# Performance work log

Hardware: AMD Instinct MI355X
Metric: run time of the kernel (lower is better)

Reference implementation:

```python
import jax, jax.numpy as jnp
import numpy as np

DIM = 512          # model dim
K = 4              # max_block_size (depthwise conv kernel size)
DS = 4             # downsample_factor
BLOCKS = (1, 2, 3, 4)  # block sizes, all offset 0
MULT = 12          # lcm(1,2,3,4) = block_pad_multiple
VOCAB = 256


def setup_inputs() -> dict:
    key = jax.random.key(0)
    ks = jax.random.split(key, 7)
    x = jax.random.randint(ks[0], (4, 4096), 0, VOCAB)
    emb = jax.random.normal(ks[1], (VOCAB, DIM), dtype=jnp.float32) * 0.02
    dw_w = jax.random.normal(ks[2], (DIM, 1, K), dtype=jnp.float32) * 0.1   # depthwise conv weight [out, in/groups, k]
    dw_b = jnp.zeros((DIM,), dtype=jnp.float32)
    pw_w = jax.random.normal(ks[3], (DIM, DIM), dtype=jnp.float32) * 0.05   # 1x1 conv weight [out, in]
    pw_b = jnp.zeros((DIM,), dtype=jnp.float32)
    score_w = jax.random.normal(ks[4], (DIM,), dtype=jnp.float32) * 0.05    # Linear(dim,1)
    score_b = jnp.zeros((), dtype=jnp.float32)
    return {"x": x, "emb": emb, "dw_w": dw_w, "dw_b": dw_b,
            "pw_w": pw_w, "pw_b": pw_b, "score_w": score_w, "score_b": score_b}


def _gbst(x, emb, dw_w, dw_b, pw_w, pw_b, score_w, score_b):
    b, n = x.shape
    m = ((n + DS - 1) // DS) * DS  # next multiple of downsample factor
    xe = emb[x]  # [b, n, d]

    # positional: Pad seq end by K-1, depthwise conv1d(k=K), then 1x1 conv
    xp = jnp.pad(xe, ((0, 0), (0, K - 1), (0, 0)))
    xc = jnp.transpose(xp, (0, 2, 1))  # [b, d, n+K-1]
    y = jax.lax.conv_general_dilated(
        xc, dw_w, window_strides=(1,), padding='VALID',
        dimension_numbers=('NCH', 'OIH', 'NCH'), feature_group_count=DIM)
    y = y + dw_b[None, :, None]                       # [b, d, n]
    y = jnp.einsum('ed,bdn->bne', pw_w, y) + pw_b     # [b, n, d]

    # pad seq to multiple of lcm of block sizes
    L = ((n + MULT - 1) // MULT) * MULT
    xpad = jnp.pad(y, ((0, 0), (0, L - n), (0, 0)))   # [b, L, d]

    # multi-scale block mean pooling, broadcast back to full length
    reprs = []
    for bs in BLOCKS:
        br = xpad.reshape(b, L // bs, bs, DIM).mean(axis=2)  # [b, L/bs, d]
        reprs.append(jnp.repeat(br, bs, axis=1))             # [b, L, d]
    block_reprs = jnp.stack(reprs, axis=2)  # [b, L, nblocks, d]

    # learned block scoring + softmax over block sizes
    scores = jnp.einsum('blkd,d->blk', block_reprs, score_w) + score_b
    scores = jax.nn.softmax(scores, axis=2)  # [b, L, nblocks]

    # consensus attention over positions (inner dim = nblocks)
    sim = jnp.einsum('bik,bjk->bij', scores, scores)  # [b, L, L]
    attn = jax.nn.softmax(sim, axis=-1)
    scores = jnp.einsum('bij,bjk->bik', attn, scores)

    out = jnp.einsum('blkd,blk->bld', block_reprs, scores)  # [b, L, d]
    out = out[:, :m]
    out = out.reshape(b, m // DS, DS, DIM).mean(axis=2)     # [b, m/DS, d]
    return out


def reference(x, emb, dw_w, dw_b, pw_w, pw_b, score_w, score_b):
    return _gbst(x, emb, dw_w, dw_b, pw_w, pw_b, score_w, score_b)
```

## Files before the change

kernel.cpp:

```cpp
#include <hip/hip_runtime.h>
#include <hip/hip_bf16.h>

#define DIMD 512
#define NSEQ 4096
#define LPAD 4104
#define NCH 12
#define CH 342
#define SPLITS 8
#define PT_BK 32

#define OFF_P      0u
#define OFF_CONST  524288u
#define OFF_T      524800u
#define OFF_S      541216u
#define OFF_AACC   606880u
#define OFF_Y      672544u
#define OFF_PPART  2773792u

static __device__ __forceinline__ unsigned short f2bf(float f) {
  unsigned u = __float_as_uint(f);
  unsigned r = (u + 0x7FFFu + ((u >> 16) & 1u)) >> 16;
  return (unsigned short)r;
}
static __device__ __forceinline__ float bf2f(unsigned short h) {
  return __uint_as_float(((unsigned)h) << 16);
}

__global__ __launch_bounds__(256) void k_ptable(
    const float* __restrict__ emb, const float* __restrict__ dw_w,
    const float* __restrict__ pw_w, float* __restrict__ Ppart) {
  __shared__ float As[PT_BK][68];
  __shared__ float Bs[PT_BK][68];
  const int tid = threadIdx.x;
  const int m0 = blockIdx.x * 64;
  const int e0 = blockIdx.y * 64;
  const int z  = blockIdx.z;
  const int kk = m0 >> 8;
  const int v0 = m0 & 255;
  const int srow = tid >> 3;
  const int sd4  = (tid & 7) * 4;
  const int ty = tid >> 4, tx = tid & 15;
  float c[4][4] = {};
  for (int kt = 0; kt < 64; kt += PT_BK) {
    const int d0 = z * 64 + kt;
    const float dw0 = dw_w[(d0 + sd4 + 0) * 4 + kk];
    const float dw1 = dw_w[(d0 + sd4 + 1) * 4 + kk];
    const float dw2 = dw_w[(d0 + sd4 + 2) * 4 + kk];
    const float dw3 = dw_w[(d0 + sd4 + 3) * 4 + kk];
    #pragma unroll
    for (int rr = 0; rr < 2; ++rr) {
      const int row = srow + rr * 32;
      float4 ev = *reinterpret_cast<const float4*>(&emb[(v0 + row) * DIMD + d0 + sd4]);
      As[sd4 + 0][row] = ev.x * dw0;
      As[sd4 + 1][row] = ev.y * dw1;
      As[sd4 + 2][row] = ev.z * dw2;
      As[sd4 + 3][row] = ev.w * dw3;
      float4 bv = *reinterpret_cast<const float4*>(&pw_w[(e0 + row) * DIMD + d0 + sd4]);
      Bs[sd4 + 0][row] = bv.x;
      Bs[sd4 + 1][row] = bv.y;
      Bs[sd4 + 2][row] = bv.z;
      Bs[sd4 + 3][row] = bv.w;
    }
    __syncthreads();
    #pragma unroll
    for (int q = 0; q < PT_BK; ++q) {
      float4 a = *reinterpret_cast<const float4*>(&As[q][ty * 4]);
      float4 b = *reinterpret_cast<const float4*>(&Bs[q][tx * 4]);
      c[0][0] += a.x * b.x; c[0][1] += a.x * b.y; c[0][2] += a.x * b.z; c[0][3] += a.x * b.w;
      c[1][0] += a.y * b.x; c[1][1] += a.y * b.y; c[1][2] += a.y * b.z; c[1][3] += a.y * b.w;
      c[2][0] += a.z * b.x; c[2][1] += a.z * b.y; c[2][2] += a.z * b.z; c[2][3] += a.z * b.w;
      c[3][0] += a.w * b.x; c[3][1] += a.w * b.y; c[3][2] += a.w * b.z; c[3][3] += a.w * b.w;
    }
    __syncthreads();
  }
  #pragma unroll
  for (int i = 0; i < 4; ++i) {
    *reinterpret_cast<float4*>(
        &Ppart[(size_t)z * 524288u + (m0 + ty * 4 + i) * DIMD + e0 + tx * 4]) =
        make_float4(c[i][0], c[i][1], c[i][2], c[i][3]);
  }
}

__global__ __launch_bounds__(256) void k_pcomb(
    const float* __restrict__ Ppart, float* __restrict__ P,
    const float* __restrict__ pw_w, const float* __restrict__ pw_b,
    const float* __restrict__ dw_b, float* __restrict__ constv) {
  const int idx = blockIdx.x * 256 + threadIdx.x;
  const float4* p4 = reinterpret_cast<const float4*>(Ppart);
  float4 a = p4[idx];
  #pragma unroll
  for (int zz = 1; zz < SPLITS; ++zz) {
    float4 v = p4[(size_t)zz * 131072u + idx];
    a.x += v.x; a.y += v.y; a.z += v.z; a.w += v.w;
  }
  reinterpret_cast<float4*>(P)[idx] = a;
  if (blockIdx.x < 2) {
    const int e = blockIdx.x * 256 + threadIdx.x;
    float acc = pw_b[e];
    const float4* pr = reinterpret_cast<const float4*>(&pw_w[e * DIMD]);
    const float4* db = reinterpret_cast<const float4*>(dw_b);
    for (int d4 = 0; d4 < DIMD / 4; ++d4) {
      float4 w = pr[d4]; float4 bb = db[d4];
      acc += w.x * bb.x + w.y * bb.y + w.z * bb.z + w.w * bb.w;
    }
    constv[e] = acc;
  }
}

__global__ __launch_bounds__(128) void k_y(
    const int* __restrict__ x, const float* __restrict__ P,
    const float* __restrict__ constv, const float* __restrict__ score_w,
    unsigned short* __restrict__ y, float* __restrict__ t_out) {
  const int b = blockIdx.y;
  const int i0 = blockIdx.x * 8;
  const int t = threadIdx.x;
  __shared__ float red[2][8];
  float4 cv = reinterpret_cast<const float4*>(constv)[t];
  float4 sw = reinterpret_cast<const float4*>(score_w)[t];
  float td[8];
  for (int r = 0; r < 8; ++r) {
    const int i = i0 + r;
    float ax = 0.f, ay = 0.f, az = 0.f, aw = 0.f;
    if (i < NSEQ) {
      ax = cv.x; ay = cv.y; az = cv.z; aw = cv.w;
      #pragma unroll
      for (int k = 0; k < 4; ++k) {
        const int pos = i + k;
        if (pos < NSEQ) {
          const int tok = x[b * NSEQ + pos];
          const float4 pv = *reinterpret_cast<const float4*>(
              &P[((unsigned)(k << 8) + tok) * DIMD + t * 4]);
          ax += pv.x; ay += pv.y; az += pv.z; aw += pv.w;
        }
      }
    }
    ushort4 o;
    o.x = f2bf(ax); o.y = f2bf(ay); o.z = f2bf(az); o.w = f2bf(aw);
    *reinterpret_cast<ushort4*>(&y[((size_t)(b * LPAD) + i) * DIMD + t * 4]) = o;
    td[r] = ax * sw.x + ay * sw.y + az * sw.z + aw * sw.w;
  }
  const int lane = t & 63, wv = t >> 6;
  #pragma unroll
  for (int r = 0; r < 8; ++r) {
    float p = td[r];
    for (int off = 32; off > 0; off >>= 1) p += __shfl_down(p, off);
    if (lane == 0) red[wv][r] = p;
  }
  __syncthreads();
  if (t < 8) t_out[b * LPAD + i0 + t] = red[0][t] + red[1][t];
}

__global__ __launch_bounds__(256) void k_s(
    const float* __restrict__ t_in, const float* __restrict__ score_b_p,
    float* __restrict__ s, float* __restrict__ Aacc) {
  const int b = blockIdx.y;
  const int l = blockIdx.x * 256 + threadIdx.x;
  if (l >= LPAD) return;
  reinterpret_cast<float4*>(Aacc)[(size_t)(b * LPAD) + l] = make_float4(0.f, 0.f, 0.f, 0.f);
  const float* tb = &t_in[b * LPAD];
  const float sb = score_b_p[0];
  float p0 = tb[l] + sb;
  int j2 = l & ~1;
  float p1 = (tb[j2] + tb[j2 + 1]) * 0.5f + sb;
  int j3 = (l / 3) * 3;
  float p2 = (tb[j3] + tb[j3 + 1] + tb[j3 + 2]) * (1.0f / 3.0f) + sb;
  int j4 = l & ~3;
  float p3 = (tb[j4] + tb[j4 + 1] + tb[j4 + 2] + tb[j4 + 3]) * 0.25f + sb;
  float mx = fmaxf(fmaxf(p0, p1), fmaxf(p2, p3));
  float e0 = __expf(p0 - mx), e1 = __expf(p1 - mx);
  float e2 = __expf(p2 - mx), e3 = __expf(p3 - mx);
  float inv = 1.0f / (e0 + e1 + e2 + e3);
  *reinterpret_cast<float4*>(&s[((size_t)(b * LPAD) + l) * 4]) =
      make_float4(e0 * inv, e1 * inv, e2 * inv, e3 * inv);
}

__global__ __launch_bounds__(256) void k_attn(
    const float* __restrict__ s, float* __restrict__ Aacc) {
  const int b = blockIdx.z;
  const int c = blockIdx.y;
  const int i = blockIdx.x * 256 + threadIdx.x;
  __shared__ float4 sch[CH];
  const float4* s4 = reinterpret_cast<const float4*>(s) + (size_t)b * LPAD;
  const int j0 = c * CH;
  for (int idx = threadIdx.x; idx < CH; idx += 256) sch[idx] = s4[j0 + idx];
  __syncthreads();
  if (i >= LPAD) return;
  float4 si = s4[i];
  float a0x = 0.f, a0y = 0.f, a0z = 0.f, a0w = 0.f;
  float a1x = 0.f, a1y = 0.f, a1z = 0.f, a1w = 0.f;
  #pragma unroll 3
  for (int jj = 0; jj < CH; jj += 2) {
    float4 u = sch[jj];
    float4 v = sch[jj + 1];
    float d0 = si.x * u.x + si.y * u.y + si.z * u.z + si.w * u.w;
    float d1 = si.x * v.x + si.y * v.y + si.z * v.z + si.w * v.w;
    float e0 = __expf(d0), e1 = __expf(d1);
    a0x += e0 * u.x; a0y += e0 * u.y; a0z += e0 * u.z; a0w += e0 * u.w;
    a1x += e1 * v.x; a1y += e1 * v.y; a1z += e1 * v.z; a1w += e1 * v.w;
  }
  float* aa = &Aacc[((size_t)(b * LPAD) + i) * 4];
  atomicAdd(aa + 0, a0x + a1x);
  atomicAdd(aa + 1, a0y + a1y);
  atomicAdd(aa + 2, a0z + a1z);
  atomicAdd(aa + 3, a0w + a1w);
}

__global__ __launch_bounds__(256) void k_out(
    const unsigned short* __restrict__ y, const float* __restrict__ Aacc,
    float* __restrict__ out) {
  const int b = blockIdx.y;
  const int h = threadIdx.x >> 7;
  const int tl = threadIdx.x & 127;
  const int g = blockIdx.x * 2 + h;
  __shared__ float coef[2][8];
  const int jbase = (g == 0) ? 0 : 4 * g - 2;
  if (tl == 0) {
    float cf[8] = {0.f, 0.f, 0.f, 0.f, 0.f, 0.f, 0.f, 0.f};
    const float4* a4 = reinterpret_cast<const float4*>(Aacc) + (size_t)b * LPAD;
    for (int dl = 0; dl < 4; ++dl) {
      int l = 4 * g + dl;
      float4 av = a4[l];
      float inv = 1.0f / (av.x + av.y + av.z + av.w);
      float sk[4] = {av.x * inv, av.y * inv, av.z * inv, av.w * inv};
      for (int k = 0; k < 4; ++k) {
        int bs = k + 1;
        int j0 = (l / bs) * bs;
        float wv = sk[k] / (float)(bs * 4);
        for (int jj = 0; jj < bs; ++jj) cf[j0 + jj - jbase] += wv;
      }
    }
    for (int r = 0; r < 8; ++r) coef[h][r] = cf[r];
  }
  __syncthreads();
  const unsigned short* yb = y + ((size_t)(b * LPAD) + jbase) * DIMD + tl * 4;
  float ax = 0.f, ay = 0.f, az = 0.f, aw = 0.f;
  #pragma unroll
  for (int r = 0; r < 8; ++r) {
    float cr = coef[h][r];
    ushort4 v = *reinterpret_cast<const ushort4*>(&yb[r * DIMD]);
    ax += cr * bf2f(v.x); ay += cr * bf2f(v.y);
    az += cr * bf2f(v.z); aw += cr * bf2f(v.w);
  }
  reinterpret_cast<float4*>(out)[((size_t)(b * 1024) + g) * 128 + tl] =
      make_float4(ax, ay, az, aw);
}

extern "C" void kernel_launch(void* const* d_in, const int* in_sizes, int n_in,
                              void* d_out, int out_size, void* d_ws, size_t ws_size,
                              hipStream_t stream) {
  const int* x = (const int*)d_in[0];
  const float* emb = (const float*)d_in[1];
  const float* dw_w = (const float*)d_in[2];
  const float* dw_b = (const float*)d_in[3];
  const float* pw_w = (const float*)d_in[4];
  const float* pw_b = (const float*)d_in[5];
  const float* score_w = (const float*)d_in[6];
  const float* score_b = (const float*)d_in[7];
  float* out = (float*)d_out;
  float* ws = (float*)d_ws;
  float* P      = ws + OFF_P;
  float* constv = ws + OFF_CONST;
  float* t      = ws + OFF_T;
  float* s      = ws + OFF_S;
  float* Aacc   = ws + OFF_AACC;
  unsigned short* y = (unsigned short*)(ws + OFF_Y);
  float* Ppart  = ws + OFF_PPART;

  k_ptable<<<dim3(16, 8, SPLITS), 256, 0, stream>>>(emb, dw_w, pw_w, Ppart);
  k_pcomb<<<512, 256, 0, stream>>>(Ppart, P, pw_w, pw_b, dw_b, constv);
  k_y<<<dim3(513, 4), 128, 0, stream>>>(x, P, constv, score_w, y, t);
  k_s<<<dim3(17, 4), 256, 0, stream>>>(t, score_b, s, Aacc);
  k_attn<<<dim3(17, NCH, 4), 256, 0, stream>>>(s, Aacc);
  k_out<<<dim3(512, 4), 256, 0, stream>>>(y, Aacc, out);
}
```

Measured before the change: 156.3 us.

## Eliminate materialized y buffer by projecting P table onto score weights

Instead of writing the full bf16 y tensor [b, L, d] and reducing it to per-position scores, the P-table rows are dotted with score_w up front to form a small q table. Per-position scores then come from four table lookups, and k_scores fuses the old k_y and k_s kernels. k_out rebuilds y on the fly from token lookups into P, which drops the large y write and read at the cost of more gathered P loads per output. As a side effect, k_out now accumulates in fp32 instead of reading bf16-rounded y.

```diff
diff --git a/kernel.cpp b/kernel.cpp
--- a/kernel.cpp
+++ b/kernel.cpp
@@ -11,20 +11,10 @@
 
 #define OFF_P      0u
 #define OFF_CONST  524288u
-#define OFF_T      524800u
-#define OFF_S      541216u
-#define OFF_AACC   606880u
-#define OFF_Y      672544u
-#define OFF_PPART  2773792u
-
-static __device__ __forceinline__ unsigned short f2bf(float f) {
-  unsigned u = __float_as_uint(f);
-  unsigned r = (u + 0x7FFFu + ((u >> 16) & 1u)) >> 16;
-  return (unsigned short)r;
-}
-static __device__ __forceinline__ float bf2f(unsigned short h) {
-  return __uint_as_float(((unsigned)h) << 16);
-}
+#define OFF_Q      524800u
+#define OFF_S      525824u
+#define OFF_AACC   591488u
+#define OFF_PPART  657152u
 
 __global__ __launch_bounds__(256) void k_ptable(
     const float* __restrict__ emb, const float* __restrict__ dw_w,
@@ -84,8 +74,11 @@
 __global__ __launch_bounds__(256) void k_pcomb(
     const float* __restrict__ Ppart, float* __restrict__ P,
     const float* __restrict__ pw_w, const float* __restrict__ pw_b,
-    const float* __restrict__ dw_b, float* __restrict__ constv) {
-  const int idx = blockIdx.x * 256 + threadIdx.x;
+    const float* __restrict__ dw_b, const float* __restrict__ score_w,
+    float* __restrict__ constv, float* __restrict__ q) {
+  __shared__ float qred[4];
+  const int tid = threadIdx.x;
+  const int idx = blockIdx.x * 256 + tid;
   const float4* p4 = reinterpret_cast<const float4*>(Ppart);
   float4 a = p4[idx];
   #pragma unroll
@@ -94,8 +87,15 @@
     a.x += v.x; a.y += v.y; a.z += v.z; a.w += v.w;
   }
   reinterpret_cast<float4*>(P)[idx] = a;
+  float4 sw = reinterpret_cast<const float4*>(score_w)[idx & 127];
+  float part = a.x * sw.x + a.y * sw.y + a.z * sw.z + a.w * sw.w;
+  for (int off = 32; off > 0; off >>= 1) part += __shfl_down(part, off);
+  if ((tid & 63) == 0) qred[tid >> 6] = part;
+  __syncthreads();
+  if (tid == 0)   q[blockIdx.x * 2 + 0] = qred[0] + qred[1];
+  if (tid == 128) q[blockIdx.x * 2 + 1] = qred[2] + qred[3];
   if (blockIdx.x < 2) {
-    const int e = blockIdx.x * 256 + threadIdx.x;
+    const int e = blockIdx.x * 256 + tid;
     float acc = pw_b[e];
     const float4* pr = reinterpret_cast<const float4*>(&pw_w[e * DIMD]);
     const float4* db = reinterpret_cast<const float4*>(dw_b);
@@ -107,65 +107,54 @@
   }
 }
 
-__global__ __launch_bounds__(128) void k_y(
-    const int* __restrict__ x, const float* __restrict__ P,
+__global__ __launch_bounds__(256) void k_scores(
+    const int* __restrict__ x, const float* __restrict__ q,
     const float* __restrict__ constv, const float* __restrict__ score_w,
-    unsigned short* __restrict__ y, float* __restrict__ t_out) {
+    const float* __restrict__ score_b_p, float* __restrict__ s,
+    float* __restrict__ Aacc) {
+  __shared__ float qlds[1024];
+  __shared__ float tlds[264];
+  __shared__ float c0red[2];
   const int b = blockIdx.y;
-  const int i0 = blockIdx.x * 8;
-  const int t = threadIdx.x;
-  __shared__ float red[2][8];
-  float4 cv = reinterpret_cast<const float4*>(constv)[t];
-  float4 sw = reinterpret_cast<const float4*>(score_w)[t];
-  float td[8];
-  for (int r = 0; r < 8; ++r) {
-    const int i = i0 + r;
-    float ax = 0.f, ay = 0.f, az = 0.f, aw = 0.f;
-    if (i < NSEQ) {
-      ax = cv.x; ay = cv.y; az = cv.z; aw = cv.w;
-      #pragma unroll
-      for (int k = 0; k < 4; ++k) {
-        const int pos = i + k;
-        if (pos < NSEQ) {
-          const int tok = x[b * NSEQ + pos];
-          const float4 pv = *reinterpret_cast<const float4*>(
-              &P[((unsigned)(k << 8) + tok) * DIMD + t * 4]);
-          ax += pv.x; ay += pv.y; az += pv.z; aw += pv.w;
-        }
-      }
-    }
-    ushort4 o;
-    o.x = f2bf(ax); o.y = f2bf(ay); o.z = f2bf(az); o.w = f2bf(aw);
-    *reinterpret_cast<ushort4*>(&y[((size_t)(b * LPAD) + i) * DIMD + t * 4]) = o;
-    td[r] = ax * sw.x + ay * sw.y + az * sw.z + aw * sw.w;
-  }
-  const int lane = t & 63, wv = t >> 6;
-  #pragma unroll
-  for (int r = 0; r < 8; ++r) {
-    float p = td[r];
-    for (int off = 32; off > 0; off >>= 1) p += __shfl_down(p, off);
-    if (lane == 0) red[wv][r] = p;
-  }
-  __syncthreads();
-  if (t < 8) t_out[b * LPAD + i0 + t] = red[0][t] + red[1][t];
-}
-
-__global__ __launch_bounds__(256) void k_s(
-    const float* __restrict__ t_in, const float* __restrict__ score_b_p,
-    float* __restrict__ s, float* __restrict__ Aacc) {
-  const int b = blockIdx.y;
-  const int l = blockIdx.x * 256 + threadIdx.x;
+  const int l0 = blockIdx.x * 256;
+  const int tid = threadIdx.x;
+  reinterpret_cast<float4*>(qlds)[tid] = reinterpret_cast<const float4*>(q)[tid];
+  if (tid < 128) {
+    float4 cv = reinterpret_cast<const float4*>(constv)[tid];
+    float4 sw = reinterpret_cast<const float4*>(score_w)[tid];
+    float part = cv.x * sw.x + cv.y * sw.y + cv.z * sw.z + cv.w * sw.w;
+    for (int off = 32; off > 0; off >>= 1) part += __shfl_down(part, off);
+    if ((tid & 63) == 0) c0red[tid >> 6] = part;
+  }
+  __syncthreads();
+  const float c0 = c0red[0] + c0red[1];
+  const int* xb = &x[b * NSEQ];
+  auto tval = [&](int l) -> float {
+    if ((unsigned)l >= (unsigned)NSEQ) return 0.f;
+    float acc = c0;
+    #pragma unroll
+    for (int k = 0; k < 4; ++k) {
+      const int pos = l + k;
+      if (pos < NSEQ) acc += qlds[(k << 8) + xb[pos]];
+    }
+    return acc;
+  };
+  tlds[tid] = tval(l0 - 2 + tid);
+  if (tid < 5) tlds[256 + tid] = tval(l0 + 254 + tid);
+  __syncthreads();
+  const int l = l0 + tid;
   if (l >= LPAD) return;
   reinterpret_cast<float4*>(Aacc)[(size_t)(b * LPAD) + l] = make_float4(0.f, 0.f, 0.f, 0.f);
-  const float* tb = &t_in[b * LPAD];
   const float sb = score_b_p[0];
-  float p0 = tb[l] + sb;
+  #define TT(j) tlds[(j) - l0 + 2]
+  float p0 = TT(l) + sb;
   int j2 = l & ~1;
-  float p1 = (tb[j2] + tb[j2 + 1]) * 0.5f + sb;
+  float p1 = (TT(j2) + TT(j2 + 1)) * 0.5f + sb;
   int j3 = (l / 3) * 3;
-  float p2 = (tb[j3] + tb[j3 + 1] + tb[j3 + 2]) * (1.0f / 3.0f) + sb;
+  float p2 = (TT(j3) + TT(j3 + 1) + TT(j3 + 2)) * (1.0f / 3.0f) + sb;
   int j4 = l & ~3;
-  float p3 = (tb[j4] + tb[j4 + 1] + tb[j4 + 2] + tb[j4 + 3]) * 0.25f + sb;
+  float p3 = (TT(j4) + TT(j4 + 1) + TT(j4 + 2) + TT(j4 + 3)) * 0.25f + sb;
+  #undef TT
   float mx = fmaxf(fmaxf(p0, p1), fmaxf(p2, p3));
   float e0 = __expf(p0 - mx), e1 = __expf(p1 - mx);
   float e2 = __expf(p2 - mx), e3 = __expf(p3 - mx);
@@ -181,11 +170,11 @@
   const int i = blockIdx.x * 256 + threadIdx.x;
   __shared__ float4 sch[CH];
   const float4* s4 = reinterpret_cast<const float4*>(s) + (size_t)b * LPAD;
+  float4 si = s4[i < LPAD ? i : 0];
   const int j0 = c * CH;
   for (int idx = threadIdx.x; idx < CH; idx += 256) sch[idx] = s4[j0 + idx];
   __syncthreads();
   if (i >= LPAD) return;
-  float4 si = s4[i];
   float a0x = 0.f, a0y = 0.f, a0z = 0.f, a0w = 0.f;
   float a1x = 0.f, a1y = 0.f, a1z = 0.f, a1w = 0.f;
   #pragma unroll 3
@@ -206,7 +195,8 @@
 }
 
 __global__ __launch_bounds__(256) void k_out(
-    const unsigned short* __restrict__ y, const float* __restrict__ Aacc,
+    const int* __restrict__ x, const float* __restrict__ P,
+    const float* __restrict__ constv, const float* __restrict__ Aacc,
     float* __restrict__ out) {
   const int b = blockIdx.y;
   const int h = threadIdx.x >> 7;
@@ -232,15 +222,29 @@
     for (int r = 0; r < 8; ++r) coef[h][r] = cf[r];
   }
   __syncthreads();
-  const unsigned short* yb = y + ((size_t)(b * LPAD) + jbase) * DIMD + tl * 4;
+  const int* xb = &x[b * NSEQ];
   float ax = 0.f, ay = 0.f, az = 0.f, aw = 0.f;
+  float csum = 0.f;
   #pragma unroll
   for (int r = 0; r < 8; ++r) {
-    float cr = coef[h][r];
-    ushort4 v = *reinterpret_cast<const ushort4*>(&yb[r * DIMD]);
-    ax += cr * bf2f(v.x); ay += cr * bf2f(v.y);
-    az += cr * bf2f(v.z); aw += cr * bf2f(v.w);
-  }
+    const int row = jbase + r;
+    if (row < NSEQ) {
+      const float cr = coef[h][r];
+      csum += cr;
+      #pragma unroll
+      for (int k = 0; k < 4; ++k) {
+        const int pos = row + k;
+        if (pos < NSEQ) {
+          const int tok = xb[pos];
+          const float4 pv = *reinterpret_cast<const float4*>(
+              &P[((unsigned)(k << 8) + tok) * DIMD + tl * 4]);
+          ax += cr * pv.x; ay += cr * pv.y; az += cr * pv.z; aw += cr * pv.w;
+        }
+      }
+    }
+  }
+  const float4 cv = reinterpret_cast<const float4*>(constv)[tl];
+  ax += csum * cv.x; ay += csum * cv.y; az += csum * cv.z; aw += csum * cv.w;
   reinterpret_cast<float4*>(out)[((size_t)(b * 1024) + g) * 128 + tl] =
       make_float4(ax, ay, az, aw);
 }
@@ -260,16 +264,14 @@
   float* ws = (float*)d_ws;
   float* P      = ws + OFF_P;
   float* constv = ws + OFF_CONST;
-  float* t      = ws + OFF_T;
+  float* q      = ws + OFF_Q;
   float* s      = ws + OFF_S;
   float* Aacc   = ws + OFF_AACC;
-  unsigned short* y = (unsigned short*)(ws + OFF_Y);
   float* Ppart  = ws + OFF_PPART;
 
   k_ptable<<<dim3(16, 8, SPLITS), 256, 0, stream>>>(emb, dw_w, pw_w, Ppart);
-  k_pcomb<<<512, 256, 0, stream>>>(Ppart, P, pw_w, pw_b, dw_b, constv);
-  k_y<<<dim3(513, 4), 128, 0, stream>>>(x, P, constv, score_w, y, t);
-  k_s<<<dim3(17, 4), 256, 0, stream>>>(t, score_b, s, Aacc);
+  k_pcomb<<<512, 256, 0, stream>>>(Ppart, P, pw_w, pw_b, dw_b, score_w, constv, q);
+  k_scores<<<dim3(17, 4), 256, 0, stream>>>(x, q, constv, score_w, score_b, s, Aacc);
   k_attn<<<dim3(17, NCH, 4), 256, 0, stream>>>(s, Aacc);
-  k_out<<<dim3(512, 4), 256, 0, stream>>>(y, Aacc, out);
-}
+  k_out<<<dim3(512, 4), 256, 0, stream>>>(x, P, constv, Aacc, out);
+}
```

After: 152.1 us. -2.6%, faster.
